# Kernel tuning notes

Measured on AMD Instinct MI355X. Metric: run time of the kernel, lower is better.

The kernel has to match this reference:

```python
import jax, jax.numpy as jnp
import numpy as np

NUM_CLASS = 4096
HIDDEN = 512
N_GROUPS = 64  # per branch (co and cl)
BATCH = 64


def _make_group_of(rng, n_groups, num_class):
    # Ragged partition of [0, num_class) into n_groups contiguous segments,
    # mirroring len_co_list_index offsets of the original module.
    cuts = np.sort(rng.choice(np.arange(1, num_class), size=n_groups - 1, replace=False))
    sizes = np.diff(np.concatenate([[0], cuts, [num_class]]))
    return np.repeat(np.arange(n_groups), sizes)  # [num_class] -> group id per class slot


def setup_inputs() -> dict:
    key = jax.random.key(0)
    k_x, k_cow, k_clw, k_cob, k_clb = jax.random.split(key, 5)
    rng = np.random.default_rng(0)
    stdv = 1.0 / np.sqrt(HIDDEN)  # matches reset_parameters uniform(-stdv, stdv)

    x = jax.random.normal(k_x, (BATCH, 2 * N_GROUPS, HIDDEN), dtype=jnp.float32)
    co_W = jax.random.uniform(k_cow, (1, NUM_CLASS, HIDDEN), jnp.float32, -stdv, stdv)
    cl_W = jax.random.uniform(k_clw, (1, NUM_CLASS, HIDDEN), jnp.float32, -stdv, stdv)
    co_b = jax.random.uniform(k_cob, (1, NUM_CLASS), jnp.float32, -stdv, stdv)
    cl_b = jax.random.uniform(k_clb, (1, NUM_CLASS), jnp.float32, -stdv, stdv)

    co_group_of = jnp.asarray(_make_group_of(rng, N_GROUPS, NUM_CLASS), jnp.int32)
    cl_group_of = jnp.asarray(_make_group_of(rng, N_GROUPS, NUM_CLASS), jnp.int32)
    # co_index / cl_index are class-id permutations applied after concat
    co_index = jnp.asarray(rng.permutation(NUM_CLASS), jnp.int32)
    cl_index = jnp.asarray(rng.permutation(NUM_CLASS), jnp.int32)

    return {
        "x": x,
        "co_W": co_W, "cl_W": cl_W,
        "co_b": co_b, "cl_b": cl_b,
        "co_group_of": co_group_of, "cl_group_of": cl_group_of,
        "co_index": co_index, "cl_index": cl_index,
        "group_len": N_GROUPS,
    }


def reference(x, co_W, cl_W, co_b, cl_b, co_group_of, cl_group_of, co_index, cl_index, group_len):
    # x: [B, 2*G, H]; first G group-features feed the co branch, rest the cl branch.
    co_x = x[:, :group_len, :]   # [B, G, H]
    cl_x = x[:, group_len:, :]   # [B, G, H]

    # Fused ragged group-wise broadcast-multiply + reduce:
    # out[b, c] = dot(W[0, c], x[b, group_of[c]]) + b[0, c]
    co_out = jnp.einsum("bch,ch->bc", co_x[:, co_group_of, :], co_W[0]) + co_b  # [B, C]
    cl_out = jnp.einsum("bch,ch->bc", cl_x[:, cl_group_of, :], cl_W[0]) + cl_b  # [B, C]

    # Final index_select gather over classes
    return co_out[:, co_index], cl_out[:, cl_index]
```

## Files before the change

kernel.cpp:

```cpp
#include <hip/hip_runtime.h>
#include <hip/hip_bf16.h>
#include <string.h>

#define NUM_CLASS 4096
#define HIDDEN    512
#define NGROUPS   64
#define BATCH     64

#define WS_INV   10240
#define TMP_OFF_F 16384
#define TMP_H_STRIDE (4096*64)
#define TMP_S_STRIDE (2*4096*64)

typedef __attribute__((ext_vector_type(8))) short short8;
typedef __attribute__((ext_vector_type(4))) float f32x4;

__device__ __forceinline__ unsigned int pack2bf(float a, float b) {
    __hip_bfloat16 ha = __float2bfloat16(a), hb = __float2bfloat16(b);
    unsigned short ua, ub;
    memcpy(&ua, &ha, 2); memcpy(&ub, &hb, 2);
    return (unsigned int)ua | ((unsigned int)ub << 16);
}

__device__ __forceinline__ short8 cvt8(float4 a, float4 b) {
    union { short8 s; unsigned int u[4]; } r;
    r.u[0] = pack2bf(a.x, a.y); r.u[1] = pack2bf(a.z, a.w);
    r.u[2] = pack2bf(b.x, b.y); r.u[3] = pack2bf(b.z, b.w);
    return r.s;
}

__global__ __launch_bounds__(1024) void prep_inv_kernel(
    const int* __restrict__ co_idx, const int* __restrict__ cl_idx,
    int* __restrict__ ws)
{
    int tid = threadIdx.x;
    for (int v = tid; v < 2 * NUM_CLASS; v += 1024) {
        int h = v >> 12, c = v & (NUM_CLASS - 1);
        const int* idx = h ? cl_idx : co_idx;
        ws[WS_INV + h * NUM_CLASS + idx[c]] = c;
    }
}

template<int KS>
__global__ __launch_bounds__(256, (KS == 1) ? 2 : 4) void gwl_gemm_direct(
    const float* __restrict__ x,
    const float* __restrict__ co_W, const float* __restrict__ cl_W,
    const int* __restrict__ co_gof, const int* __restrict__ cl_gof,
    float* __restrict__ tmp)
{
    const int KQ = 16 / KS;
    const int nblk = 256 * KS;
    const int chunk = nblk >> 3;
    int bid = blockIdx.x;
    int swz = (bid & 7) * chunk + (bid >> 3);
    int cid = swz & 63;
    int r1  = swz >> 6;
    int h   = r1 & 1;
    int r2  = r1 >> 1;
    int kh  = r2 & (KS - 1);
    int bs  = r2 >> ((KS == 1) ? 0 : (KS == 2) ? 1 : 2);
    int c0  = cid * 64;

    const float* Wp  = h ? cl_W : co_W;
    const int*   gof = h ? cl_gof : co_gof;

    int tid = threadIdx.x;
    int l = tid & 63, w = tid >> 6;
    int kcol  = kh * (HIDDEN / KS) + (l >> 4) * 8;
    int crow  = c0 + w * 16 + (l & 15);
    int bbase = bs * 32 + (l & 15);

    short8 bfrag[KQ];
    #pragma unroll
    for (int kq = 0; kq < KQ; ++kq) {
        const float* wp = Wp + (size_t)crow * 512 + kcol + kq * 32;
        bfrag[kq] = cvt8(*(const float4*)wp, *(const float4*)(wp + 4));
    }

    int gl = gof[crow];
    float* tmph = tmp + (size_t)(kh * 2 + h) * TMP_H_STRIDE;

    unsigned int pend = 0xFFFFu;
    while (pend) {
        int slot0 = (int)__builtin_ctz(pend);
        int g = __shfl(gl, slot0);
        unsigned long long eq = __ballot(gl == g);
        pend &= ~(unsigned int)(eq & 0xFFFFu);

        int xr = h * 64 + g;
        const float* xp = x + (size_t)xr * 512 + kcol;

        f32x4 acc0 = (f32x4)(0.0f), acc1 = (f32x4)(0.0f);
        #pragma unroll
        for (int kp = 0; kp < KQ; kp += 2) {
            float4 f[8];
            #pragma unroll
            for (int kq2 = 0; kq2 < 2; ++kq2)
                #pragma unroll
                for (int i = 0; i < 2; ++i) {
                    const float* ap = xp + (size_t)(bbase + i * 16) * 65536
                                    + (kp + kq2) * 32;
                    f[(kq2 * 2 + i) * 2]     = *(const float4*)ap;
                    f[(kq2 * 2 + i) * 2 + 1] = *(const float4*)(ap + 4);
                }
            #pragma unroll
            for (int kq2 = 0; kq2 < 2; ++kq2) {
                short8 a0 = cvt8(f[(kq2 * 2 + 0) * 2], f[(kq2 * 2 + 0) * 2 + 1]);
                short8 a1 = cvt8(f[(kq2 * 2 + 1) * 2], f[(kq2 * 2 + 1) * 2 + 1]);
                acc0 = __builtin_amdgcn_mfma_f32_16x16x32_bf16(
                           a0, bfrag[kp + kq2], acc0, 0, 0, 0);
                acc1 = __builtin_amdgcn_mfma_f32_16x16x32_bf16(
                           a1, bfrag[kp + kq2], acc1, 0, 0, 0);
            }
        }

        if (gl == g) {
            float* tr = tmph + (size_t)crow * 64 + bs * 32 + (l >> 4) * 4;
            *(f32x4*)(tr)      = acc0;
            *(f32x4*)(tr + 16) = acc1;
        }
    }
}

template<int KS>
__global__ __launch_bounds__(256) void gwl_permute32(
    const float* __restrict__ tmp,
    const float* __restrict__ co_b, const float* __restrict__ cl_b,
    const int* __restrict__ co_idx, const int* __restrict__ cl_idx,
    float* __restrict__ out)
{
    int jc = blockIdx.x;
    int h  = blockIdx.y;
    const float* bias = h ? cl_b : co_b;
    const int*   idx  = h ? cl_idx : co_idx;
    const float* tmph = tmp + (size_t)h * TMP_H_STRIDE;

    __shared__ float tile[64][33];
    int tid = threadIdx.x;
    int lane = tid & 63, w = tid >> 6;

    #pragma unroll
    for (int u = 0; u < 8; ++u) {
        int jj = u * 4 + w;
        int j  = jc * 32 + jj;
        int c  = idx[j];
        float v = bias[c];
        #pragma unroll
        for (int s = 0; s < KS; ++s)
            v += tmph[(size_t)s * TMP_S_STRIDE + (size_t)c * 64 + lane];
        tile[lane][jj] = v;
    }
    __syncthreads();

    #pragma unroll
    for (int p = 0; p < 2; ++p) {
        int f = p * 256 + tid;
        int b = f >> 3, j4 = (f & 7) * 4;
        *(float4*)&out[((size_t)h * 64 + b) * 4096 + jc * 32 + j4] =
            *(const float4*)&tile[b][j4];
    }
}

__global__ __launch_bounds__(256, 4) void gwl_stage1_scatter(
    const float* __restrict__ x,
    const float* __restrict__ co_W, const float* __restrict__ cl_W,
    const float* __restrict__ co_b, const float* __restrict__ cl_b,
    const int* __restrict__ co_gof, const int* __restrict__ cl_gof,
    int* __restrict__ ws, float* __restrict__ out)
{
    const int NCH = 8;
    const int nblk = 128;
    const int chunk = nblk >> 3;
    int bid = blockIdx.x;
    int swz = (bid & 7) * chunk + (bid >> 3);
    int cid = swz & 63;
    int h   = swz >> 6;
    int c0  = cid * 64;

    const float* Wp  = h ? cl_W : co_W;
    const int*   gof = h ? cl_gof : co_gof;

    __shared__ __align__(16) unsigned short Xs[64][72];
    __shared__ __align__(16) unsigned short Wls[64][72];
    __shared__ float ftile[64][65];
    __shared__ int s_seg_lo[65];
    __shared__ int s_seg_g[64];
    __shared__ int s_nseg;

    int tid = threadIdx.x;
    int l = tid & 63, w = tid >> 6;

    if (tid < 64) {
        int gi = gof[c0 + tid];
        int prev = (tid == 0) ? -1 : gof[c0 + tid - 1];
        bool is_start = (gi != prev);
        unsigned long long m = __ballot(is_start);
        int segidx = (int)__popcll(m & ((1ull << tid) - 1ull));
        if (is_start) { s_seg_lo[segidx] = tid; s_seg_g[segidx] = gi; }
        if (tid == 0) {
            int ns = (int)__popcll(m);
            s_nseg = ns;
            s_seg_lo[ns] = 64;
        }
    }

    int rowq[4], kvq[4];
    #pragma unroll
    for (int q = 0; q < 4; ++q) {
        int v = q * 256 + tid;
        rowq[q] = v >> 4;
        kvq[q]  = v & 15;
    }

    float4 rxA[4], rwA[4], rxB[4], rwB[4];
    f32x4 acc[4];
    #pragma unroll
    for (int i = 0; i < 4; ++i) acc[i] = (f32x4)(0.0f);

#define LOADC(S, RX, RW) do {                                                       \
    int si_ = (S) / NCH, t_ = (S) % NCH;                                            \
    int k0_ = t_ * 64;                                                              \
    int xr_ = h * 64 + s_seg_g[si_];                                                \
    _Pragma("unroll")                                                               \
    for (int q = 0; q < 4; ++q) {                                                   \
        RX[q] = *(const float4*)(x + rowq[q] * 65536 + xr_ * 512 + k0_ + kvq[q]*4); \
        RW[q] = *(const float4*)(Wp + (c0 + rowq[q]) * 512 + k0_ + kvq[q] * 4);     \
    } } while (0)

#define STOREC(RX, RW) do {                                                         \
    _Pragma("unroll")                                                               \
    for (int q = 0; q < 4; ++q) {                                                   \
        unsigned int x0 = pack2bf(RX[q].x, RX[q].y);                                \
        unsigned int x1 = pack2bf(RX[q].z, RX[q].w);                                \
        *(uint2*)&Xs[rowq[q]][kvq[q] * 4] = make_uint2(x0, x1);                     \
        unsigned int w0 = pack2bf(RW[q].x, RW[q].y);                                \
        unsigned int w1 = pack2bf(RW[q].z, RW[q].w);                                \
        *(uint2*)&Wls[rowq[q]][kvq[q] * 4] = make_uint2(w0, w1);                    \
    } } while (0)

#define COMPUTEC() do {                                                             \
    _Pragma("unroll")                                                               \
    for (int kq = 0; kq < 2; ++kq) {                                                \
        int koff = kq * 32 + (l >> 4) * 8;                                          \
        short8 bfrag = *(const short8*)&Wls[w * 16 + (l & 15)][koff];               \
        _Pragma("unroll")                                                           \
        for (int i = 0; i < 4; ++i) {                                               \
            short8 afrag = *(const short8*)&Xs[16 * i + (l & 15)][koff];            \
            acc[i] = __builtin_amdgcn_mfma_f32_16x16x32_bf16(afrag, bfrag, acc[i],  \
                                                             0, 0, 0);              \
        }                                                                           \
    } } while (0)

    __syncthreads();
    int nseg = s_nseg;
    int nsteps = nseg * NCH;
    int slotw = w * 16 + (l & 15);

    LOADC(0, rxA, rwA);
    STOREC(rxA, rwA);
    __syncthreads();

    #pragma unroll 1
    for (int s = 0; s < nsteps; ++s) {
        bool nxt = (s + 1 < nsteps);
        if (nxt) {
            if (s & 1) LOADC(s + 1, rxA, rwA);
            else       LOADC(s + 1, rxB, rwB);
        }
        COMPUTEC();
        if ((s % NCH) == NCH - 1) {
            int si = s / NCH;
            int lo = s_seg_lo[si], hi = s_seg_lo[si + 1];
            if (slotw >= lo && slotw < hi) {
                #pragma unroll
                for (int i = 0; i < 4; ++i)
                    #pragma unroll
                    for (int r = 0; r < 4; ++r)
                        ftile[slotw][16 * i + (l >> 4) * 4 + r] = acc[i][r];
            }
            #pragma unroll
            for (int i = 0; i < 4; ++i) acc[i] = (f32x4)(0.0f);
        }
        __syncthreads();
        if (nxt) {
            if (s & 1) STOREC(rxA, rwA);
            else       STOREC(rxB, rwB);
            __syncthreads();
        }
    }

    const float* bias = h ? cl_b : co_b;
    const int*   inv  = ws + WS_INV + h * NUM_CLASS;
    float* outh = out + (size_t)h * BATCH * NUM_CLASS;
    #pragma unroll
    for (int p = 0; p < 4; ++p) {
        int f = p * 256 + tid;
        int slot = f >> 4, b4 = (f & 15) * 4;
        int c = c0 + slot;
        int oc = inv[c];
        float bb = bias[c];
        #pragma unroll
        for (int e = 0; e < 4; ++e)
            outh[(b4 + e) * 4096 + oc] = ftile[slot][b4 + e] + bb;
    }
#undef LOADC
#undef STOREC
#undef COMPUTEC
}

extern "C" void kernel_launch(void* const* d_in, const int* in_sizes, int n_in,
                              void* d_out, int out_size, void* d_ws, size_t ws_size,
                              hipStream_t stream)
{
    (void)in_sizes; (void)n_in; (void)out_size;
    const float* x      = (const float*)d_in[0];
    const float* co_W   = (const float*)d_in[1];
    const float* cl_W   = (const float*)d_in[2];
    const float* co_b   = (const float*)d_in[3];
    const float* cl_b   = (const float*)d_in[4];
    const int*   co_gof = (const int*)d_in[5];
    const int*   cl_gof = (const int*)d_in[6];
    const int*   co_idx = (const int*)d_in[7];
    const int*   cl_idx = (const int*)d_in[8];
    int*   ws  = (int*)d_ws;
    float* tmp = (float*)d_ws + TMP_OFF_F;
    float* out = (float*)d_out;

    const size_t base  = (size_t)TMP_OFF_F * 4;
    const size_t slice = (size_t)TMP_S_STRIDE * 4;

    if (ws_size >= base + 4 * slice) {
        hipLaunchKernelGGL((gwl_gemm_direct<4>), dim3(1024), dim3(256), 0, stream,
                           x, co_W, cl_W, co_gof, cl_gof, tmp);
        hipLaunchKernelGGL((gwl_permute32<4>), dim3(128, 2), dim3(256), 0, stream,
                           tmp, co_b, cl_b, co_idx, cl_idx, out);
    } else if (ws_size >= base + 2 * slice) {
        hipLaunchKernelGGL((gwl_gemm_direct<2>), dim3(512), dim3(256), 0, stream,
                           x, co_W, cl_W, co_gof, cl_gof, tmp);
        hipLaunchKernelGGL((gwl_permute32<2>), dim3(128, 2), dim3(256), 0, stream,
                           tmp, co_b, cl_b, co_idx, cl_idx, out);
    } else if (ws_size >= base + 1 * slice) {
        hipLaunchKernelGGL((gwl_gemm_direct<1>), dim3(256), dim3(256), 0, stream,
                           x, co_W, cl_W, co_gof, cl_gof, tmp);
        hipLaunchKernelGGL((gwl_permute32<1>), dim3(128, 2), dim3(256), 0, stream,
                           tmp, co_b, cl_b, co_idx, cl_idx, out);
    } else {
        hipLaunchKernelGGL(prep_inv_kernel, dim3(1), dim3(1024), 0, stream,
                           co_idx, cl_idx, ws);
        hipLaunchKernelGGL(gwl_stage1_scatter, dim3(128), dim3(256), 0, stream,
                           x, co_W, cl_W, co_b, cl_b, co_gof, cl_gof, ws, out);
    }
}
```

Baseline: 26.96 us.

## Cover full batch per GEMM block and hoist index/bias loads in permute

Each gemm_direct block now computes all 64 batch rows, using four MFMA accumulators instead of two, rather than splitting the batch in halves. This halves the grid and reuses the converted W fragments across twice as many batch rows, cutting redundant W loads and conversions. The cost is fewer blocks for latency hiding, plus more register pressure from 16 float4 staging loads. The permute kernel also loads all indices and biases up front so those loads can overlap.

```diff
diff --git a/kernel.cpp b/kernel.cpp
--- a/kernel.cpp
+++ b/kernel.cpp
@@ -49,16 +49,14 @@
     float* __restrict__ tmp)
 {
     const int KQ = 16 / KS;
-    const int nblk = 256 * KS;
+    const int nblk = 128 * KS;
     const int chunk = nblk >> 3;
     int bid = blockIdx.x;
     int swz = (bid & 7) * chunk + (bid >> 3);
     int cid = swz & 63;
     int r1  = swz >> 6;
     int h   = r1 & 1;
-    int r2  = r1 >> 1;
-    int kh  = r2 & (KS - 1);
-    int bs  = r2 >> ((KS == 1) ? 0 : (KS == 2) ? 1 : 2);
+    int kh  = r1 >> 1;
     int c0  = cid * 64;
 
     const float* Wp  = h ? cl_W : co_W;
@@ -68,8 +66,9 @@
     int l = tid & 63, w = tid >> 6;
     int kcol  = kh * (HIDDEN / KS) + (l >> 4) * 8;
     int crow  = c0 + w * 16 + (l & 15);
-    int bbase = bs * 32 + (l & 15);
-
+    int brow  = l & 15;
+
+    int gl = gof[crow];
     short8 bfrag[KQ];
     #pragma unroll
     for (int kq = 0; kq < KQ; ++kq) {
@@ -77,7 +76,6 @@
         bfrag[kq] = cvt8(*(const float4*)wp, *(const float4*)(wp + 4));
     }
 
-    int gl = gof[crow];
     float* tmph = tmp + (size_t)(kh * 2 + h) * TMP_H_STRIDE;
 
     unsigned int pend = 0xFFFFu;
@@ -90,34 +88,38 @@
         int xr = h * 64 + g;
         const float* xp = x + (size_t)xr * 512 + kcol;
 
-        f32x4 acc0 = (f32x4)(0.0f), acc1 = (f32x4)(0.0f);
+        f32x4 acc[4];
+        #pragma unroll
+        for (int i = 0; i < 4; ++i) acc[i] = (f32x4)(0.0f);
+
         #pragma unroll
         for (int kp = 0; kp < KQ; kp += 2) {
-            float4 f[8];
+            float4 f[16];
             #pragma unroll
             for (int kq2 = 0; kq2 < 2; ++kq2)
                 #pragma unroll
-                for (int i = 0; i < 2; ++i) {
-                    const float* ap = xp + (size_t)(bbase + i * 16) * 65536
+                for (int i = 0; i < 4; ++i) {
+                    const float* ap = xp + (size_t)(brow + i * 16) * 65536
                                     + (kp + kq2) * 32;
-                    f[(kq2 * 2 + i) * 2]     = *(const float4*)ap;
-                    f[(kq2 * 2 + i) * 2 + 1] = *(const float4*)(ap + 4);
+                    f[(kq2 * 4 + i) * 2]     = *(const float4*)ap;
+                    f[(kq2 * 4 + i) * 2 + 1] = *(const float4*)(ap + 4);
                 }
             #pragma unroll
-            for (int kq2 = 0; kq2 < 2; ++kq2) {
-                short8 a0 = cvt8(f[(kq2 * 2 + 0) * 2], f[(kq2 * 2 + 0) * 2 + 1]);
-                short8 a1 = cvt8(f[(kq2 * 2 + 1) * 2], f[(kq2 * 2 + 1) * 2 + 1]);
-                acc0 = __builtin_amdgcn_mfma_f32_16x16x32_bf16(
-                           a0, bfrag[kp + kq2], acc0, 0, 0, 0);
-                acc1 = __builtin_amdgcn_mfma_f32_16x16x32_bf16(
-                           a1, bfrag[kp + kq2], acc1, 0, 0, 0);
-            }
+            for (int kq2 = 0; kq2 < 2; ++kq2)
+                #pragma unroll
+                for (int i = 0; i < 4; ++i) {
+                    short8 af = cvt8(f[(kq2 * 4 + i) * 2],
+                                     f[(kq2 * 4 + i) * 2 + 1]);
+                    acc[i] = __builtin_amdgcn_mfma_f32_16x16x32_bf16(
+                                 af, bfrag[kp + kq2], acc[i], 0, 0, 0);
+                }
         }
 
         if (gl == g) {
-            float* tr = tmph + (size_t)crow * 64 + bs * 32 + (l >> 4) * 4;
-            *(f32x4*)(tr)      = acc0;
-            *(f32x4*)(tr + 16) = acc1;
+            float* tr = tmph + (size_t)crow * 64 + (l >> 4) * 4;
+            #pragma unroll
+            for (int i = 0; i < 4; ++i)
+                *(f32x4*)(tr + 16 * i) = acc[i];
         }
     }
 }
@@ -139,15 +141,20 @@
     int tid = threadIdx.x;
     int lane = tid & 63, w = tid >> 6;
 
+    int cc[8];
+    #pragma unroll
+    for (int u = 0; u < 8; ++u) cc[u] = idx[jc * 32 + u * 4 + w];
+    float bb[8];
+    #pragma unroll
+    for (int u = 0; u < 8; ++u) bb[u] = bias[cc[u]];
+
     #pragma unroll
     for (int u = 0; u < 8; ++u) {
         int jj = u * 4 + w;
-        int j  = jc * 32 + jj;
-        int c  = idx[j];
-        float v = bias[c];
+        float v = bb[u];
         #pragma unroll
         for (int s = 0; s < KS; ++s)
-            v += tmph[(size_t)s * TMP_S_STRIDE + (size_t)c * 64 + lane];
+            v += tmph[(size_t)s * TMP_S_STRIDE + (size_t)cc[u] * 64 + lane];
         tile[lane][jj] = v;
     }
     __syncthreads();
@@ -169,10 +176,8 @@
     int* __restrict__ ws, float* __restrict__ out)
 {
     const int NCH = 8;
-    const int nblk = 128;
-    const int chunk = nblk >> 3;
     int bid = blockIdx.x;
-    int swz = (bid & 7) * chunk + (bid >> 3);
+    int swz = (bid & 7) * 16 + (bid >> 3);
     int cid = swz & 63;
     int h   = swz >> 6;
     int c0  = cid * 64;
@@ -330,17 +335,17 @@
     const size_t slice = (size_t)TMP_S_STRIDE * 4;
 
     if (ws_size >= base + 4 * slice) {
-        hipLaunchKernelGGL((gwl_gemm_direct<4>), dim3(1024), dim3(256), 0, stream,
+        hipLaunchKernelGGL((gwl_gemm_direct<4>), dim3(512), dim3(256), 0, stream,
                            x, co_W, cl_W, co_gof, cl_gof, tmp);
         hipLaunchKernelGGL((gwl_permute32<4>), dim3(128, 2), dim3(256), 0, stream,
                            tmp, co_b, cl_b, co_idx, cl_idx, out);
     } else if (ws_size >= base + 2 * slice) {
-        hipLaunchKernelGGL((gwl_gemm_direct<2>), dim3(512), dim3(256), 0, stream,
+        hipLaunchKernelGGL((gwl_gemm_direct<2>), dim3(256), dim3(256), 0, stream,
                            x, co_W, cl_W, co_gof, cl_gof, tmp);
         hipLaunchKernelGGL((gwl_permute32<2>), dim3(128, 2), dim3(256), 0, stream,
                            tmp, co_b, cl_b, co_idx, cl_idx, out);
     } else if (ws_size >= base + 1 * slice) {
-        hipLaunchKernelGGL((gwl_gemm_direct<1>), dim3(256), dim3(256), 0, stream,
+        hipLaunchKernelGGL((gwl_gemm_direct<1>), dim3(128), dim3(256), 0, stream,
                            x, co_W, cl_W, co_gof, cl_gof, tmp);
         hipLaunchKernelGGL((gwl_permute32<1>), dim3(128, 2), dim3(256), 0, stream,
                            tmp, co_b, cl_b, co_idx, cl_idx, out);
```

New measurement: 31.68 us. 1.18x slower.
